# Kernel tuning notes

Hardware: AMD Instinct MI355X
Metric: run time of the kernel (lower is better)

Reference implementation:

```python
import jax, jax.numpy as jnp
import numpy as np

B, N, E = 16, 10000, 160000
C_IN, C_SP, C_OUT = 32, 16, 32


def _glorot(key, shape):
    s = float(np.sqrt(6.0 / (shape[0] + shape[1])))
    return jax.random.uniform(key, shape, jnp.float32, -s, s)


def setup_inputs() -> dict:
    key = jax.random.key(0)
    ks = jax.random.split(key, 12)
    X = jax.random.normal(ks[0], (B, N, C_IN), jnp.float32)
    edge_index1 = jax.random.randint(ks[1], (2, E), 0, N)
    edge_weight1 = jax.random.uniform(ks[2], (E,), jnp.float32)
    res_n_id1 = jnp.arange(N)
    edge_index2 = jax.random.randint(ks[3], (2, E), 0, N)
    edge_weight2 = jax.random.uniform(ks[4], (E,), jnp.float32)
    res_n_id2 = jnp.arange(N)
    # conv1 params (in=C_IN, out=C_SP, edge_channels=1, concat=True)
    amp_w1 = _glorot(ks[5], (1, C_IN))            # [edge_ch, in]
    gate_w1 = _glorot(ks[6], (2 * C_IN + 1, 1))   # Linear(2*in+edge_ch, 1)
    gate_b1 = jnp.zeros((1,), jnp.float32)
    w1 = _glorot(ks[7], (2 * C_IN, C_SP))         # concat weight
    b1 = jnp.zeros((C_SP,), jnp.float32)
    # conv2 params (in=C_SP, out=C_OUT)
    amp_w2 = _glorot(ks[8], (1, C_SP))
    gate_w2 = _glorot(ks[9], (2 * C_SP + 1, 1))
    gate_b2 = jnp.zeros((1,), jnp.float32)
    w2 = _glorot(ks[10], (2 * C_SP, C_OUT))
    b2 = jnp.zeros((C_OUT,), jnp.float32)
    return dict(X=X, edge_index1=edge_index1, edge_weight1=edge_weight1, res_n_id1=res_n_id1,
                edge_index2=edge_index2, edge_weight2=edge_weight2, res_n_id2=res_n_id2,
                amp_w1=amp_w1, gate_w1=gate_w1, gate_b1=gate_b1, w1=w1, b1=b1,
                amp_w2=amp_w2, gate_w2=gate_w2, gate_b2=gate_b2, w2=w2, b2=b2)


def _sagela(x_src, x_dst, edge_index, edge_weight, amp_w, gate_w, gate_b, w, b):
    # x_src: [B, N_src, C], x_dst: [B, N_dst, C]
    src, dst = edge_index[0], edge_index[1]
    n_dst = x_dst.shape[1]
    C = x_src.shape[-1]
    x_j = x_src[:, src]                       # [B, E, C] gathered source feats
    x_i = x_dst[:, dst]                       # [B, E, C] gathered target feats
    e = edge_weight[:, None]                  # [E, 1] edge features
    # gate_linear(cat[x_i, x_j, e]) split into three matmuls (same math)
    wg_i, wg_j, wg_e = gate_w[:C], gate_w[C:2 * C], gate_w[2 * C:]
    lamb = jax.nn.sigmoid(x_i @ wg_i + x_j @ wg_j + (e @ wg_e)[None] + gate_b)  # [B, E, 1]
    amp = e @ amp_w                           # [E, C] edge amplification
    msg = amp[None, :, :] * x_j * lamb        # [B, E, C]
    # mean aggregation over incoming edges (scatter-add / count)
    aggr = jnp.zeros((x_src.shape[0], n_dst, C), msg.dtype).at[:, dst].add(msg)
    cnt = jnp.zeros((n_dst,), msg.dtype).at[dst].add(1.0)
    aggr = aggr / jnp.maximum(cnt, 1.0)[None, :, None]
    out = jnp.concatenate([x_dst, aggr], axis=-1) @ w + b  # [B, N_dst, out]
    return out


def reference(X, edge_index1, edge_weight1, res_n_id1, edge_index2, edge_weight2, res_n_id2,
              amp_w1, gate_w1, gate_b1, w1, b1, amp_w2, gate_w2, gate_b2, w2, b2):
    h = _sagela(X, X[:, res_n_id1], edge_index1, edge_weight1, amp_w1, gate_w1, gate_b1, w1, b1)
    h = jax.nn.leaky_relu(h, 0.01)
    out = _sagela(h, h[:, res_n_id2], edge_index2, edge_weight2, amp_w2, gate_w2, gate_b2, w2, b2)
    return out
```

## Files before the change

### kernel.cpp

```cpp
#include <hip/hip_runtime.h>
#include <math.h>

#define B 16
#define N 10000
#define E 160000
#define CAP 64

__device__ __forceinline__ ushort f2bf(float v) {
    uint u = __float_as_uint(v);
    u = (u + 0x7fffu + ((u >> 16) & 1u)) >> 16;
    return (ushort)u;
}
__device__ __forceinline__ float bf2f(ushort u) { return __uint_as_float(((uint)u) << 16); }
__device__ __forceinline__ float bf2f_lo(uint u) { return __uint_as_float(u << 16); }
__device__ __forceinline__ float bf2f_hi(uint u) { return __uint_as_float(u & 0xffff0000u); }
__device__ __forceinline__ float dec_ew(uint u) {
    return ((float)(u >> 14) + 0.5f) * (1.0f / 262144.0f);
}

__global__ __launch_bounds__(256, 8)
void prep_fused_kernel(const float* __restrict__ X,
                       const float* __restrict__ gate_w1,
                       const float* __restrict__ amp_w1,
                       const float* __restrict__ b1,
                       const int* __restrict__ ei1, const float* __restrict__ ew1,
                       const int* __restrict__ ei2, const float* __restrict__ ew2,
                       const float* __restrict__ w1,
                       ushort* __restrict__ yt,
                       float* __restrict__ xpart,
                       float* __restrict__ gi, float* __restrict__ gj,
                       int* __restrict__ bcount1, uint* __restrict__ bucket1,
                       int* __restrict__ bcount2, uint* __restrict__ bucket2) {
    __shared__ __align__(16) float s_w1[64 * 16];
    __shared__ float s_x[16][33];
    __shared__ float s_py[16][17];

    int tid = threadIdx.x;
    int gtid = blockIdx.x * 256 + tid;

    if (gtid < 2 * E) {
        if (gtid < E) {
            int t = gtid;
            int d = ei1[E + t];
            int pos = atomicAdd(&bcount1[d], 1);
            if (pos < CAP) {
                uint q = (uint)(ew1[t] * 262144.0f);
                if (q > 262143u) q = 262143u;
                bucket1[d * CAP + pos] = (q << 14) | (uint)ei1[t];
            }
        } else {
            int e = gtid - E;
            int d = ei2[E + e];
            int pos = atomicAdd(&bcount2[d], 1);
            if (pos < CAP) {
                uint q = (uint)(ew2[e] * 262144.0f);
                if (q > 262143u) q = 262143u;
                bucket2[d * CAP + pos] = (q << 14) | (uint)ei2[e];
            }
        }
    }

    {
        int i = tid * 4;
        *(float4*)&s_w1[i] = *(const float4*)&w1[i];
    }
    int b = tid >> 4, o = tid & 15;
    for (int n = blockIdx.x; n < N; n += gridDim.x) {
        __syncthreads();
        {
            int bb = tid >> 4, c2 = (tid & 15) * 2;
            float2 v = *(const float2*)(X + ((size_t)bb * N + n) * 32 + c2);
            s_x[bb][c2] = v.x; s_x[bb][c2 + 1] = v.y;
        }
        __syncthreads();

        float po = b1[o], py = 0.f;
        #pragma unroll
        for (int c = 0; c < 32; ++c) {
            float xa = s_x[b][c];
            po += xa * s_w1[c * 16 + o];
            py += amp_w1[c] * xa * s_w1[(32 + c) * 16 + o];
        }
        float pi = s_x[b][o] * gate_w1[o]      + s_x[b][o + 16] * gate_w1[o + 16];
        float pj = s_x[b][o] * gate_w1[32 + o] + s_x[b][o + 16] * gate_w1[48 + o];
        #pragma unroll
        for (int off = 8; off; off >>= 1) {
            pi += __shfl_xor(pi, off, 16);
            pj += __shfl_xor(pj, off, 16);
        }
        int r = n * 16 + b;
        xpart[(size_t)r * 16 + o] = po;
        s_py[b][o] = py;
        if (o == 0) { gi[r] = pi; gj[r] = pj; }
        __syncthreads();

        if (tid < 64) {
            int bb = tid >> 2, j = tid & 3;
            uint lo = (uint)f2bf(s_py[bb][4 * j])     | ((uint)f2bf(s_py[bb][4 * j + 1]) << 16);
            uint hi = (uint)f2bf(s_py[bb][4 * j + 2]) | ((uint)f2bf(s_py[bb][4 * j + 3]) << 16);
            ((uint2*)yt)[(size_t)(n * 16 + bb) * 4 + j] = make_uint2(lo, hi);
        }
    }
}

__global__ __launch_bounds__(256, 8)
void agg1_kernel(const uint4* __restrict__ y4,
                 const float* __restrict__ xpart,
                 const float* __restrict__ gi,
                 const float* __restrict__ gj,
                 const int* __restrict__ bcount,
                 const uint* __restrict__ bucket,
                 const float* __restrict__ gate_w,
                 const float* __restrict__ gate_b,
                 const float* __restrict__ gate_w2,
                 ushort* __restrict__ htb,
                 float* __restrict__ gi2, float* __restrict__ gj2) {
    int tid = threadIdx.x;
    const int nb = N / 4;
    int bg = blockIdx.x / nb;
    int n0 = (blockIdx.x - bg * nb) * 4;
    int wv = tid >> 6, l = tid & 63;
    int n = n0 + wv;
    int og = l & 1, bl = (l >> 1) & 7, h = l >> 4;
    int b = bg * 8 + bl;

    int cnt = bcount[n];
    int deg = cnt < CAP ? cnt : CAP;
    float wge = gate_w[64];
    float gib = gi[n * 16 + b] + gate_b[0];
    uint my_pr = bucket[(size_t)n * CAP + l];

    float a0 = 0.f, a1 = 0.f, a2 = 0.f, a3 = 0.f;
    float a4 = 0.f, a5 = 0.f, a6 = 0.f, a7 = 0.f;
    for (int k = h; k < deg; k += 8) {
        int k1 = k + 4;
        bool v1 = k1 < deg;
        uint pr0 = __shfl(my_pr, k, 64);
        uint pr1 = __shfl(my_pr, v1 ? k1 : k, 64);
        uint s0 = pr0 & 0x3FFFu, s1 = pr1 & 0x3FFFu;
        float g0 = gj[s0 * 16 + b];
        float g1 = gj[s1 * 16 + b];
        uint4 u0 = y4[s0 * 32u + (uint)b * 2u + og];
        uint4 u1 = y4[s1 * 32u + (uint)b * 2u + og];
        float w0 = dec_ew(pr0), w1 = dec_ew(pr1);
        float c0 = w0 / (1.0f + __expf(-(gib + g0 + w0 * wge)));
        float c1 = v1 ? (w1 / (1.0f + __expf(-(gib + g1 + w1 * wge)))) : 0.f;
        a0 += c0 * bf2f_lo(u0.x) + c1 * bf2f_lo(u1.x);
        a1 += c0 * bf2f_hi(u0.x) + c1 * bf2f_hi(u1.x);
        a2 += c0 * bf2f_lo(u0.y) + c1 * bf2f_lo(u1.y);
        a3 += c0 * bf2f_hi(u0.y) + c1 * bf2f_hi(u1.y);
        a4 += c0 * bf2f_lo(u0.z) + c1 * bf2f_lo(u1.z);
        a5 += c0 * bf2f_hi(u0.z) + c1 * bf2f_hi(u1.z);
        a6 += c0 * bf2f_lo(u0.w) + c1 * bf2f_lo(u1.w);
        a7 += c0 * bf2f_hi(u0.w) + c1 * bf2f_hi(u1.w);
    }
    a0 += __shfl_xor(a0, 16, 64); a0 += __shfl_xor(a0, 32, 64);
    a1 += __shfl_xor(a1, 16, 64); a1 += __shfl_xor(a1, 32, 64);
    a2 += __shfl_xor(a2, 16, 64); a2 += __shfl_xor(a2, 32, 64);
    a3 += __shfl_xor(a3, 16, 64); a3 += __shfl_xor(a3, 32, 64);
    a4 += __shfl_xor(a4, 16, 64); a4 += __shfl_xor(a4, 32, 64);
    a5 += __shfl_xor(a5, 16, 64); a5 += __shfl_xor(a5, 32, 64);
    a6 += __shfl_xor(a6, 16, 64); a6 += __shfl_xor(a6, 32, 64);
    a7 += __shfl_xor(a7, 16, 64); a7 += __shfl_xor(a7, 32, 64);

    if (h == 0) {
        float inv = 1.0f / fmaxf((float)cnt, 1.0f);
        size_t xb = ((size_t)n * 16 + b) * 16 + 8 * og;
        float4 xp0 = *(const float4*)&xpart[xb];
        float4 xp1 = *(const float4*)&xpart[xb + 4];
        float v0 = xp0.x + inv * a0, v1 = xp0.y + inv * a1;
        float v2 = xp0.z + inv * a2, v3 = xp0.w + inv * a3;
        float v4 = xp1.x + inv * a4, v5 = xp1.y + inv * a5;
        float v6 = xp1.z + inv * a6, v7 = xp1.w + inv * a7;
        v0 = v0 > 0.f ? v0 : 0.01f * v0;  v1 = v1 > 0.f ? v1 : 0.01f * v1;
        v2 = v2 > 0.f ? v2 : 0.01f * v2;  v3 = v3 > 0.f ? v3 : 0.01f * v3;
        v4 = v4 > 0.f ? v4 : 0.01f * v4;  v5 = v5 > 0.f ? v5 : 0.01f * v5;
        v6 = v6 > 0.f ? v6 : 0.01f * v6;  v7 = v7 > 0.f ? v7 : 0.01f * v7;
        uint4 pk;
        pk.x = (uint)f2bf(v0) | ((uint)f2bf(v1) << 16);
        pk.y = (uint)f2bf(v2) | ((uint)f2bf(v3) << 16);
        pk.z = (uint)f2bf(v4) | ((uint)f2bf(v5) << 16);
        pk.w = (uint)f2bf(v6) | ((uint)f2bf(v7) << 16);
        ((uint4*)htb)[(size_t)n * 32 + b * 2 + og] = pk;
        int ob = 8 * og;
        float pi = v0 * gate_w2[ob]     + v1 * gate_w2[ob + 1]
                 + v2 * gate_w2[ob + 2] + v3 * gate_w2[ob + 3]
                 + v4 * gate_w2[ob + 4] + v5 * gate_w2[ob + 5]
                 + v6 * gate_w2[ob + 6] + v7 * gate_w2[ob + 7];
        float pj = v0 * gate_w2[16 + ob]     + v1 * gate_w2[16 + ob + 1]
                 + v2 * gate_w2[16 + ob + 2] + v3 * gate_w2[16 + ob + 3]
                 + v4 * gate_w2[16 + ob + 4] + v5 * gate_w2[16 + ob + 5]
                 + v6 * gate_w2[16 + ob + 6] + v7 * gate_w2[16 + ob + 7];
        pi += __shfl_xor(pi, 1, 64);
        pj += __shfl_xor(pj, 1, 64);
        if (og == 0) { gi2[n * 16 + b] = pi; gj2[n * 16 + b] = pj; }
    }
}

__global__ __launch_bounds__(256, 8)
void agg2_kernel(const uint4* __restrict__ htb4,
                 const float* __restrict__ gi,
                 const float* __restrict__ gj,
                 const int* __restrict__ bcount,
                 const uint* __restrict__ bucket,
                 const float* __restrict__ gate_w,
                 const float* __restrict__ gate_b,
                 const float* __restrict__ amp_w,
                 const float* __restrict__ w2,
                 const float* __restrict__ b2,
                 float* __restrict__ out) {
    __shared__ __align__(16) float s_w2[32 * 36];
    __shared__ __align__(16) float s_in[4][8][36];

    int tid = threadIdx.x;
    const int nb = N / 4;
    int bg = blockIdx.x / nb;
    int n0 = (blockIdx.x - bg * nb) * 4;

    {
        int kk = tid >> 3, o4g = tid & 7;
        *(float4*)&s_w2[kk * 36 + 4 * o4g] = *(const float4*)&w2[kk * 32 + 4 * o4g];
    }
    if (tid < 64) {
        int nl = tid >> 4, idx = tid & 15;
        uint4 u = htb4[(size_t)(n0 + nl) * 32 + bg * 16 + idx];
        int bl = idx >> 1, cb = (idx & 1) * 8;
        float4 f0, f1;
        f0.x = bf2f_lo(u.x); f0.y = bf2f_hi(u.x);
        f0.z = bf2f_lo(u.y); f0.w = bf2f_hi(u.y);
        f1.x = bf2f_lo(u.z); f1.y = bf2f_hi(u.z);
        f1.z = bf2f_lo(u.w); f1.w = bf2f_hi(u.w);
        *(float4*)&s_in[nl][bl][cb]     = f0;
        *(float4*)&s_in[nl][bl][cb + 4] = f1;
    }
    __syncthreads();

    int wv = tid >> 6, l = tid & 63;
    int n = n0 + wv;
    int og = l & 1, bl = (l >> 1) & 7, q = l >> 4;
    int b = bg * 8 + bl;
    int cnt = bcount[n];
    int deg = cnt < CAP ? cnt : CAP;
    float wge = gate_w[32];
    float gib = gi[n * 16 + b] + gate_b[0];
    uint my_pr = bucket[(size_t)n * CAP + l];

    float a0 = 0.f, a1 = 0.f, a2 = 0.f, a3 = 0.f;
    float a4 = 0.f, a5 = 0.f, a6 = 0.f, a7 = 0.f;
    for (int k = q; k < deg; k += 8) {
        int k1 = k + 4;
        bool v1 = k1 < deg;
        uint pr0 = __shfl(my_pr, k, 64);
        uint pr1 = __shfl(my_pr, v1 ? k1 : k, 64);
        uint s0 = pr0 & 0x3FFFu, s1 = pr1 & 0x3FFFu;
        float g0 = gj[s0 * 16 + b];
        float g1 = gj[s1 * 16 + b];
        uint4 u0 = htb4[s0 * 32u + (uint)b * 2u + og];
        uint4 u1 = htb4[s1 * 32u + (uint)b * 2u + og];
        float w0 = dec_ew(pr0), w1 = dec_ew(pr1);
        float c0 = w0 / (1.0f + __expf(-(gib + g0 + w0 * wge)));
        float c1 = v1 ? (w1 / (1.0f + __expf(-(gib + g1 + w1 * wge)))) : 0.f;
        a0 += c0 * bf2f_lo(u0.x) + c1 * bf2f_lo(u1.x);
        a1 += c0 * bf2f_hi(u0.x) + c1 * bf2f_hi(u1.x);
        a2 += c0 * bf2f_lo(u0.y) + c1 * bf2f_lo(u1.y);
        a3 += c0 * bf2f_hi(u0.y) + c1 * bf2f_hi(u1.y);
        a4 += c0 * bf2f_lo(u0.z) + c1 * bf2f_lo(u1.z);
        a5 += c0 * bf2f_hi(u0.z) + c1 * bf2f_hi(u1.z);
        a6 += c0 * bf2f_lo(u0.w) + c1 * bf2f_lo(u1.w);
        a7 += c0 * bf2f_hi(u0.w) + c1 * bf2f_hi(u1.w);
    }
    a0 += __shfl_xor(a0, 16, 64); a0 += __shfl_xor(a0, 32, 64);
    a1 += __shfl_xor(a1, 16, 64); a1 += __shfl_xor(a1, 32, 64);
    a2 += __shfl_xor(a2, 16, 64); a2 += __shfl_xor(a2, 32, 64);
    a3 += __shfl_xor(a3, 16, 64); a3 += __shfl_xor(a3, 32, 64);
    a4 += __shfl_xor(a4, 16, 64); a4 += __shfl_xor(a4, 32, 64);
    a5 += __shfl_xor(a5, 16, 64); a5 += __shfl_xor(a5, 32, 64);
    a6 += __shfl_xor(a6, 16, 64); a6 += __shfl_xor(a6, 32, 64);
    a7 += __shfl_xor(a7, 16, 64); a7 += __shfl_xor(a7, 32, 64);
    if (q == 0) {
        float inv = 1.0f / fmaxf((float)cnt, 1.0f);
        int cb = 8 * og;
        float4 f0, f1;
        f0.x = a0 * amp_w[cb]     * inv;  f0.y = a1 * amp_w[cb + 1] * inv;
        f0.z = a2 * amp_w[cb + 2] * inv;  f0.w = a3 * amp_w[cb + 3] * inv;
        f1.x = a4 * amp_w[cb + 4] * inv;  f1.y = a5 * amp_w[cb + 5] * inv;
        f1.z = a6 * amp_w[cb + 6] * inv;  f1.w = a7 * amp_w[cb + 7] * inv;
        *(float4*)&s_in[wv][bl][16 + cb]     = f0;
        *(float4*)&s_in[wv][bl][16 + cb + 4] = f1;
    }
    __syncthreads();

    {
        int o4 = tid & 7, bl2 = (tid >> 3) & 7, nl = tid >> 6;
        float4 acc = *(const float4*)&b2[4 * o4];
        #pragma unroll
        for (int k4 = 0; k4 < 8; ++k4) {
            float4 iv = *(const float4*)&s_in[nl][bl2][4 * k4];
            float4 w0 = *(const float4*)&s_w2[(4 * k4)     * 36 + 4 * o4];
            float4 w1 = *(const float4*)&s_w2[(4 * k4 + 1) * 36 + 4 * o4];
            float4 wv2 = *(const float4*)&s_w2[(4 * k4 + 2) * 36 + 4 * o4];
            float4 w3 = *(const float4*)&s_w2[(4 * k4 + 3) * 36 + 4 * o4];
            acc.x += iv.x * w0.x + iv.y * w1.x + iv.z * wv2.x + iv.w * w3.x;
            acc.y += iv.x * w0.y + iv.y * w1.y + iv.z * wv2.y + iv.w * w3.y;
            acc.z += iv.x * w0.z + iv.y * w1.z + iv.z * wv2.z + iv.w * w3.z;
            acc.w += iv.x * w0.w + iv.y * w1.w + iv.z * wv2.w + iv.w * w3.w;
        }
        size_t ob = ((size_t)(bg * 8 + bl2) * N + (n0 + nl)) * 32;
        *(float4*)(out + ob + 4 * o4) = acc;
    }
}

extern "C" void kernel_launch(void* const* d_in, const int* in_sizes, int n_in,
                              void* d_out, int out_size, void* d_ws, size_t ws_size,
                              hipStream_t stream) {
    const float* X       = (const float*)d_in[0];
    const int*   ei1     = (const int*)  d_in[1];
    const float* ew1     = (const float*)d_in[2];
    const int*   ei2     = (const int*)  d_in[4];
    const float* ew2     = (const float*)d_in[5];
    const float* amp_w1  = (const float*)d_in[7];
    const float* gate_w1 = (const float*)d_in[8];
    const float* gate_b1 = (const float*)d_in[9];
    const float* w1      = (const float*)d_in[10];
    const float* b1      = (const float*)d_in[11];
    const float* amp_w2  = (const float*)d_in[12];
    const float* gate_w2 = (const float*)d_in[13];
    const float* gate_b2 = (const float*)d_in[14];
    const float* w2      = (const float*)d_in[15];
    const float* b2      = (const float*)d_in[16];
    float* out = (float*)d_out;

    char* p = (char*)d_ws;
    ushort* yt     = (ushort*)p; p += (size_t)N * B * 16 * sizeof(ushort);
    ushort* htb    = (ushort*)p; p += (size_t)N * B * 16 * sizeof(ushort);
    float* xpart   = (float*)p;  p += (size_t)N * B * 16 * sizeof(float);
    float* gi1     = (float*)p;  p += (size_t)N * B * sizeof(float);
    float* gj1     = (float*)p;  p += (size_t)N * B * sizeof(float);
    float* gi2     = (float*)p;  p += (size_t)N * B * sizeof(float);
    float* gj2     = (float*)p;  p += (size_t)N * B * sizeof(float);
    uint*  bucket1 = (uint*)p;   p += (size_t)N * CAP * sizeof(uint);
    uint*  bucket2 = (uint*)p;   p += (size_t)N * CAP * sizeof(uint);
    int*   bcount1 = (int*)p;    p += (size_t)N * sizeof(int);
    int*   bcount2 = (int*)p;    p += (size_t)N * sizeof(int);

    hipMemsetAsync(bcount1, 0, 2 * (size_t)N * sizeof(int), stream);
    prep_fused_kernel<<<2048, 256, 0, stream>>>(
        X, gate_w1, amp_w1, b1, ei1, ew1, ei2, ew2, w1,
        yt, xpart, gi1, gj1,
        bcount1, bucket1, bcount2, bucket2);

    agg1_kernel<<<2 * (N / 4), 256, 0, stream>>>(
        (const uint4*)yt, xpart, gi1, gj1, bcount1, bucket1,
        gate_w1, gate_b1, gate_w2, htb, gi2, gj2);

    agg2_kernel<<<2 * (N / 4), 256, 0, stream>>>(
        (const uint4*)htb, gi2, gj2, bcount2, bucket2,
        gate_w2, gate_b2, amp_w2, w2, b2, out);
}
```

Measured before the change: 173.2 us.

## Process four nodes per prep iteration and pad bucket counters to cachelines

The prep kernel now handles four nodes per loop iteration. It loads X with float4 and reuses each weight read across four accumulators, which amortizes the shared-memory weight loads and the barriers. The per-destination atomic counters are spread out with a 16-int stride so each counter sits in its own 64-byte line, reducing atomic contention between neighbouring nodes. In exchange the counter arrays and their memset are 16x larger, and the agg kernels read the counters with a strided access pattern.

```diff
diff --git a/kernel.cpp b/kernel.cpp
--- a/kernel.cpp
+++ b/kernel.cpp
@@ -5,6 +5,7 @@
 #define N 10000
 #define E 160000
 #define CAP 64
+#define CPAD 16
 
 __device__ __forceinline__ ushort f2bf(float v) {
     uint u = __float_as_uint(v);
@@ -32,8 +33,8 @@
                        int* __restrict__ bcount1, uint* __restrict__ bucket1,
                        int* __restrict__ bcount2, uint* __restrict__ bucket2) {
     __shared__ __align__(16) float s_w1[64 * 16];
-    __shared__ float s_x[16][33];
-    __shared__ float s_py[16][17];
+    __shared__ __align__(16) float s_x4[4][16][33];
+    __shared__ float s_py4[4][16][17];
 
     int tid = threadIdx.x;
     int gtid = blockIdx.x * 256 + tid;
@@ -42,7 +43,7 @@
         if (gtid < E) {
             int t = gtid;
             int d = ei1[E + t];
-            int pos = atomicAdd(&bcount1[d], 1);
+            int pos = atomicAdd(&bcount1[d * CPAD], 1);
             if (pos < CAP) {
                 uint q = (uint)(ew1[t] * 262144.0f);
                 if (q > 262143u) q = 262143u;
@@ -51,7 +52,7 @@
         } else {
             int e = gtid - E;
             int d = ei2[E + e];
-            int pos = atomicAdd(&bcount2[d], 1);
+            int pos = atomicAdd(&bcount2[d * CPAD], 1);
             if (pos < CAP) {
                 uint q = (uint)(ew2[e] * 262144.0f);
                 if (q > 262143u) q = 262143u;
@@ -65,40 +66,63 @@
         *(float4*)&s_w1[i] = *(const float4*)&w1[i];
     }
     int b = tid >> 4, o = tid & 15;
-    for (int n = blockIdx.x; n < N; n += gridDim.x) {
+    const int NG = N / 4;
+    for (int g = blockIdx.x; g < NG; g += gridDim.x) {
+        int n4 = g * 4;
         __syncthreads();
         {
-            int bb = tid >> 4, c2 = (tid & 15) * 2;
-            float2 v = *(const float2*)(X + ((size_t)bb * N + n) * 32 + c2);
-            s_x[bb][c2] = v.x; s_x[bb][c2 + 1] = v.y;
+            int sb = tid >> 4, q16 = tid & 15;
+            const float4* src = (const float4*)(X + ((size_t)sb * N + n4) * 32 + q16 * 8);
+            float4 v0 = src[0], v1 = src[1];
+            int nl = q16 >> 2, c0 = (q16 & 3) * 8;
+            *(float4*)&s_x4[nl][sb][c0]     = v0;
+            *(float4*)&s_x4[nl][sb][c0 + 4] = v1;
         }
         __syncthreads();
 
-        float po = b1[o], py = 0.f;
+        float po0 = b1[o], po1 = b1[o], po2 = b1[o], po3 = b1[o];
+        float py0 = 0.f, py1 = 0.f, py2 = 0.f, py3 = 0.f;
         #pragma unroll
         for (int c = 0; c < 32; ++c) {
-            float xa = s_x[b][c];
-            po += xa * s_w1[c * 16 + o];
-            py += amp_w1[c] * xa * s_w1[(32 + c) * 16 + o];
-        }
-        float pi = s_x[b][o] * gate_w1[o]      + s_x[b][o + 16] * gate_w1[o + 16];
-        float pj = s_x[b][o] * gate_w1[32 + o] + s_x[b][o + 16] * gate_w1[48 + o];
+            float wpo = s_w1[c * 16 + o];
+            float wpy = amp_w1[c] * s_w1[(32 + c) * 16 + o];
+            float x0 = s_x4[0][b][c], x1 = s_x4[1][b][c];
+            float x2 = s_x4[2][b][c], x3 = s_x4[3][b][c];
+            po0 += x0 * wpo; po1 += x1 * wpo; po2 += x2 * wpo; po3 += x3 * wpo;
+            py0 += x0 * wpy; py1 += x1 * wpy; py2 += x2 * wpy; py3 += x3 * wpy;
+        }
+        float gwa = gate_w1[o], gwb = gate_w1[o + 16];
+        float gwc = gate_w1[32 + o], gwd = gate_w1[48 + o];
         #pragma unroll
-        for (int off = 8; off; off >>= 1) {
-            pi += __shfl_xor(pi, off, 16);
-            pj += __shfl_xor(pj, off, 16);
-        }
-        int r = n * 16 + b;
-        xpart[(size_t)r * 16 + o] = po;
-        s_py[b][o] = py;
-        if (o == 0) { gi[r] = pi; gj[r] = pj; }
+        for (int nl = 0; nl < 4; ++nl) {
+            float xa = s_x4[nl][b][o], xb = s_x4[nl][b][o + 16];
+            float pi = xa * gwa + xb * gwb;
+            float pj = xa * gwc + xb * gwd;
+            #pragma unroll
+            for (int off = 8; off; off >>= 1) {
+                pi += __shfl_xor(pi, off, 16);
+                pj += __shfl_xor(pj, off, 16);
+            }
+            if (o == 0) {
+                int r = (n4 + nl) * 16 + b;
+                gi[r] = pi; gj[r] = pj;
+            }
+        }
+        xpart[(size_t)((n4 + 0) * 16 + b) * 16 + o] = po0;
+        xpart[(size_t)((n4 + 1) * 16 + b) * 16 + o] = po1;
+        xpart[(size_t)((n4 + 2) * 16 + b) * 16 + o] = po2;
+        xpart[(size_t)((n4 + 3) * 16 + b) * 16 + o] = po3;
+        s_py4[0][b][o] = py0; s_py4[1][b][o] = py1;
+        s_py4[2][b][o] = py2; s_py4[3][b][o] = py3;
         __syncthreads();
 
-        if (tid < 64) {
-            int bb = tid >> 2, j = tid & 3;
-            uint lo = (uint)f2bf(s_py[bb][4 * j])     | ((uint)f2bf(s_py[bb][4 * j + 1]) << 16);
-            uint hi = (uint)f2bf(s_py[bb][4 * j + 2]) | ((uint)f2bf(s_py[bb][4 * j + 3]) << 16);
-            ((uint2*)yt)[(size_t)(n * 16 + bb) * 4 + j] = make_uint2(lo, hi);
+        {
+            int nl = tid >> 6, bb = (tid >> 2) & 15, j = tid & 3;
+            uint lo = (uint)f2bf(s_py4[nl][bb][4 * j])
+                    | ((uint)f2bf(s_py4[nl][bb][4 * j + 1]) << 16);
+            uint hi = (uint)f2bf(s_py4[nl][bb][4 * j + 2])
+                    | ((uint)f2bf(s_py4[nl][bb][4 * j + 3]) << 16);
+            ((uint2*)yt)[(size_t)((n4 + nl) * 16 + bb) * 4 + j] = make_uint2(lo, hi);
         }
     }
 }
@@ -124,7 +148,7 @@
     int og = l & 1, bl = (l >> 1) & 7, h = l >> 4;
     int b = bg * 8 + bl;
 
-    int cnt = bcount[n];
+    int cnt = bcount[n * CPAD];
     int deg = cnt < CAP ? cnt : CAP;
     float wge = gate_w[64];
     float gib = gi[n * 16 + b] + gate_b[0];
@@ -239,7 +263,7 @@
     int n = n0 + wv;
     int og = l & 1, bl = (l >> 1) & 7, q = l >> 4;
     int b = bg * 8 + bl;
-    int cnt = bcount[n];
+    int cnt = bcount[n * CPAD];
     int deg = cnt < CAP ? cnt : CAP;
     float wge = gate_w[32];
     float gib = gi[n * 16 + b] + gate_b[0];
@@ -340,10 +364,10 @@
     float* gj2     = (float*)p;  p += (size_t)N * B * sizeof(float);
     uint*  bucket1 = (uint*)p;   p += (size_t)N * CAP * sizeof(uint);
     uint*  bucket2 = (uint*)p;   p += (size_t)N * CAP * sizeof(uint);
-    int*   bcount1 = (int*)p;    p += (size_t)N * sizeof(int);
-    int*   bcount2 = (int*)p;    p += (size_t)N * sizeof(int);
-
-    hipMemsetAsync(bcount1, 0, 2 * (size_t)N * sizeof(int), stream);
+    int*   bcount1 = (int*)p;    p += (size_t)N * CPAD * sizeof(int);
+    int*   bcount2 = (int*)p;    p += (size_t)N * CPAD * sizeof(int);
+
+    hipMemsetAsync(bcount1, 0, 2 * (size_t)N * CPAD * sizeof(int), stream);
     prep_fused_kernel<<<2048, 256, 0, stream>>>(
         X, gate_w1, amp_w1, b1, ei1, ew1, ei2, ew2, w1,
         yt, xpart, gi1, gj1,
```

Result: slower. 342.0 us (+97.5%).
